# Kernel optimization log

Measured on AMD Instinct MI355X. Metric: run time of the kernel, lower is better.

Reference implementation:

```python
import jax, jax.numpy as jnp
import numpy as np

B, S, D, H, DFF = 2, 2048, 768, 12, 3072
HD = D // H
LN_EPS = 1e-5


def _layernorm(x, g, b):
    mu = jnp.mean(x, axis=-1, keepdims=True)
    var = jnp.mean((x - mu) ** 2, axis=-1, keepdims=True)
    return (x - mu) * jax.lax.rsqrt(var + LN_EPS) * g + b


def setup_inputs() -> dict:
    key = jax.random.key(0)
    ks = jax.random.split(key, 16)
    s_d = 1.0 / np.sqrt(D)
    s_ff = 1.0 / np.sqrt(DFF)
    return {
        "x": jax.random.normal(ks[0], (B, S, D), jnp.float32),
        "alibi_bias": jax.random.normal(ks[1], (H, S, S), jnp.float32) * 0.1,
        "Wq": jax.random.normal(ks[2], (D, D), jnp.float32) * s_d,
        "bq": jnp.zeros((D,), jnp.float32),
        "Wk": jax.random.normal(ks[3], (D, D), jnp.float32) * s_d,
        "bk": jnp.zeros((D,), jnp.float32),
        "Wv": jax.random.normal(ks[4], (D, D), jnp.float32) * s_d,
        "bv": jnp.zeros((D,), jnp.float32),
        "Wo": jax.random.normal(ks[5], (D, D), jnp.float32) * s_d,
        "bo": jnp.zeros((D,), jnp.float32),
        "W1": jax.random.normal(ks[6], (D, DFF), jnp.float32) * s_d,
        "b1": jnp.zeros((DFF,), jnp.float32),
        "W2": jax.random.normal(ks[7], (DFF, D), jnp.float32) * s_ff,
        "b2": jnp.zeros((D,), jnp.float32),
        "g1": jnp.ones((D,), jnp.float32),
        "be1": jnp.zeros((D,), jnp.float32),
        "g2": jnp.ones((D,), jnp.float32),
        "be2": jnp.zeros((D,), jnp.float32),
    }


def reference(x, alibi_bias, Wq, bq, Wk, bk, Wv, bv, Wo, bo, W1, b1, W2, b2, g1, be1, g2, be2):
    # QKV projections -> (B, H, S, HD)
    def split_heads(t):
        return t.reshape(B, S, H, HD).transpose(0, 2, 1, 3)

    q = split_heads(x @ Wq + bq)
    k = split_heads(x @ Wk + bk)
    v = split_heads(x @ Wv + bv)

    # causal mask (S, S): -inf above diagonal
    causal = jnp.where(jnp.triu(jnp.ones((S, S), bool), k=1), -jnp.inf, 0.0).astype(x.dtype)
    mask = alibi_bias[None] + causal[None, None]  # (1, H, S, S) broadcast over batch

    scale = 1.0 / np.sqrt(HD)
    scores = jnp.einsum("bhqd,bhkd->bhqk", q, k) * scale + mask
    probs = jax.nn.softmax(scores, axis=-1)
    attn = jnp.einsum("bhqk,bhkd->bhqd", probs, v)  # (B, H, S, HD)
    attn = attn.transpose(0, 2, 1, 3).reshape(B, S, D)
    attn = attn @ Wo + bo

    x = _layernorm(x + attn, g1, be1)
    ff = jax.nn.relu(x @ W1 + b1) @ W2 + b2
    x = _layernorm(x + ff, g2, be2)
    return x
```

## Files before the change

### kernel.cpp

```cpp
#include <hip/hip_runtime.h>
#include <hip/hip_bf16.h>

#define BB 2
#define SS 2048
#define DD 768
#define HH 12
#define HD 64
#define DFF 3072
#define NROW (BB * SS)
#define QLD  2304
#define LN_EPS 1e-5f

typedef __attribute__((ext_vector_type(8))) short bf16x8;
typedef __attribute__((ext_vector_type(4))) short bf16x4;
typedef __attribute__((ext_vector_type(4))) float f32x4;

__device__ __forceinline__ void gll16(const void* g, void* l) {
    __builtin_amdgcn_global_load_lds(
        (const __attribute__((address_space(1))) unsigned int*)g,
        (__attribute__((address_space(3))) unsigned int*)l,
        16, 0, 0);
}

__device__ __forceinline__ unsigned short bf16bits(float f) {
    __hip_bfloat16 h = __float2bfloat16(f);
    return *(unsigned short*)&h;
}

__device__ __forceinline__ float bf16tof(unsigned short u) {
    unsigned int ui = ((unsigned int)u) << 16;
    return __uint_as_float(ui);
}

__device__ __forceinline__ float block_sum(float v, float* red) {
    __syncthreads();
    #pragma unroll
    for (int off = 32; off > 0; off >>= 1) v += __shfl_down(v, off, 64);
    if ((threadIdx.x & 63) == 0) red[threadIdx.x >> 6] = v;
    __syncthreads();
    if (threadIdx.x == 0) red[0] = red[0] + red[1] + red[2] + red[3];
    __syncthreads();
    return red[0];
}

template<int TM, int TN>
__global__ __launch_bounds__(256) void mfma_gemm(
        const __hip_bfloat16* __restrict__ A, const __hip_bfloat16* __restrict__ BT,
        const float* __restrict__ bias, float* __restrict__ Cf,
        __hip_bfloat16* __restrict__ Cb,
        int N, int K, int relu, int bf16out, int qscale_cols) {
    constexpr int BK = 32;
    constexpr int MW = TM / 32;
    constexpr int NW = TN / 32;
    __shared__ __hip_bfloat16 a_s[TM * BK];
    __shared__ __hip_bfloat16 b_s[TN * BK];

    const int tid  = threadIdx.x;
    const int lane = tid & 63;
    const int wid  = tid >> 6;
    const int wm   = (wid & 1) * (TM / 2);
    const int wn   = (wid >> 1) * (TN / 2);
    const int qq   = lane & 15;
    const int quad = lane >> 4;
    const int m0 = blockIdx.y * TM;
    const int n0 = blockIdx.x * TN;

    const int srow = lane >> 2;
    const int scol = (lane & 3) * 8;

    f32x4 acc[MW][NW] = {};

    for (int k0 = 0; k0 < K; k0 += BK) {
        const __hip_bfloat16* Ag = A + (size_t)m0 * K + k0 + scol;
        #pragma unroll
        for (int i = 0; i < TM / 64; i++) {
            const int row = i * 64 + wid * 16 + srow;
            gll16(Ag + (size_t)row * K, a_s + row * BK + scol);
        }
        const __hip_bfloat16* Bg = BT + (size_t)n0 * K + k0 + scol;
        #pragma unroll
        for (int i = 0; i < TN / 64; i++) {
            const int row = i * 64 + wid * 16 + srow;
            gll16(Bg + (size_t)row * K, b_s + row * BK + scol);
        }
        __syncthreads();

        bf16x8 af[MW], bfr[NW];
        #pragma unroll
        for (int mi = 0; mi < MW; mi++)
            af[mi] = *(const bf16x8*)(a_s + (wm + mi * 16 + qq) * BK + quad * 8);
        #pragma unroll
        for (int ni = 0; ni < NW; ni++)
            bfr[ni] = *(const bf16x8*)(b_s + (wn + ni * 16 + qq) * BK + quad * 8);
        #pragma unroll
        for (int mi = 0; mi < MW; mi++)
            #pragma unroll
            for (int ni = 0; ni < NW; ni++)
                acc[mi][ni] = __builtin_amdgcn_mfma_f32_16x16x32_bf16(
                        af[mi], bfr[ni], acc[mi][ni], 0, 0, 0);
        __syncthreads();
    }

    #pragma unroll
    for (int mi = 0; mi < MW; mi++) {
        #pragma unroll
        for (int ni = 0; ni < NW; ni++) {
            const int col = n0 + wn + ni * 16 + qq;
            const float bv = bias[col];
            const float sc = (col < qscale_cols) ? 0.125f : 1.0f;
            #pragma unroll
            for (int r = 0; r < 4; r++) {
                const int row = m0 + wm + mi * 16 + quad * 4 + r;
                float v = acc[mi][ni][r] + bv;
                if (relu) v = fmaxf(v, 0.f);
                v *= sc;
                if (bf16out) Cb[(size_t)row * N + col] = __float2bfloat16(v);
                else         Cf[(size_t)row * N + col] = v;
            }
        }
    }
}

__global__ __launch_bounds__(256) void transpose_bf16_kernel(
        const float* __restrict__ in, __hip_bfloat16* __restrict__ out,
        int K, int N) {
    __shared__ float t[32][33];
    const int n0 = blockIdx.x * 32;
    const int k0 = blockIdx.y * 32;
    const int r = threadIdx.x >> 3;
    const int c = threadIdx.x & 7;
    float4 v = *(const float4*)&in[(size_t)(k0 + r) * N + n0 + c * 4];
    t[r][c * 4 + 0] = v.x;
    t[r][c * 4 + 1] = v.y;
    t[r][c * 4 + 2] = v.z;
    t[r][c * 4 + 3] = v.w;
    __syncthreads();
    union { unsigned short u[4]; uint2 w; } pk;
    #pragma unroll
    for (int j = 0; j < 4; j++) pk.u[j] = bf16bits(t[c * 4 + j][r]);
    *(uint2*)&out[(size_t)(n0 + r) * K + k0 + c * 4] = pk.w;
}

__global__ __launch_bounds__(256) void cvt_bf16_kernel(
        const float* __restrict__ in, __hip_bfloat16* __restrict__ out) {
    const int i = blockIdx.x * 256 + threadIdx.x;
    float4 v = ((const float4*)in)[i];
    union { unsigned short u[4]; uint2 w; } pk;
    pk.u[0] = bf16bits(v.x); pk.u[1] = bf16bits(v.y);
    pk.u[2] = bf16bits(v.z); pk.u[3] = bf16bits(v.w);
    ((uint2*)out)[i] = pk.w;
}

__global__ __launch_bounds__(256) void concat_bias_kernel(
        const float* __restrict__ bq, const float* __restrict__ bk,
        const float* __restrict__ bv, float* __restrict__ o) {
    const int i = blockIdx.x * 256 + threadIdx.x;
    if (i < QLD)
        o[i] = (i < DD) ? bq[i] : ((i < 2 * DD) ? bk[i - DD] : bv[i - 2 * DD]);
}

__global__ __launch_bounds__(256) void flash_attn_kernel(
        const __hip_bfloat16* __restrict__ QKV, const float* __restrict__ alibi,
        __hip_bfloat16* __restrict__ Opart, float* __restrict__ ml) {
    const int qt = (int)(gridDim.x >> 1) - 1 - (int)(blockIdx.x >> 1);
    const int s  = blockIdx.x & 1;
    const int h  = blockIdx.y;
    const int b  = blockIdx.z;
    const int tid  = threadIdx.x;
    const int lane = tid & 63;
    const int w    = tid >> 6;
    const int qq   = lane & 15;
    const int quad = lane >> 4;
    const int q0   = qt * 64;

    __shared__ unsigned short K_s[64 * 72];
    __shared__ unsigned short V_t[64 * 72];
    __shared__ unsigned short al_q[64 * 72];
    __shared__ unsigned short P_t[4][16 * 72];

    const size_t qrow = ((size_t)(b * SS + q0 + w * 16 + qq)) * QLD + (size_t)h * HD;
    const bf16x8 qf0 = *(const bf16x8*)(QKV + qrow + quad * 8);
    const bf16x8 qf1 = *(const bf16x8*)(QKV + qrow + 32 + quad * 8);

    f32x4 O[4] = {};
    float m_i = -1e30f, l_i = 0.f;

    const float* alrow = alibi + ((size_t)h * SS + q0) * SS;
    const size_t kvrow0 = (size_t)(b * SS) * QLD + (size_t)h * HD + w * 16;
    const int lim = q0 + w * 16 + qq;

    for (int t = s; t * 64 <= q0; t += 2) {
        const int k0 = t * 64;
        __syncthreads();

        {
            const size_t kv = kvrow0 + (size_t)(k0 + lane) * QLD;
            bf16x8 kv0 = *(const bf16x8*)(QKV + DD + kv);
            bf16x8 kv1 = *(const bf16x8*)(QKV + DD + kv + 8);
            *(bf16x8*)&K_s[lane * 72 + w * 16]     = kv0;
            *(bf16x8*)&K_s[lane * 72 + w * 16 + 8] = kv1;
            bf16x8 vv0 = *(const bf16x8*)(QKV + 2 * DD + kv);
            bf16x8 vv1 = *(const bf16x8*)(QKV + 2 * DD + kv + 8);
            #pragma unroll
            for (int j = 0; j < 8; j++) {
                V_t[(w * 16 + j) * 72 + lane]     = vv0[j];
                V_t[(w * 16 + 8 + j) * 72 + lane] = vv1[j];
            }
            const float* ap = alrow + (size_t)lane * SS + k0 + w * 16;
            union { unsigned short u[8]; bf16x8 v; } pa0, pa1;
            float4 f0 = *(const float4*)(ap);
            float4 f1 = *(const float4*)(ap + 4);
            float4 f2 = *(const float4*)(ap + 8);
            float4 f3 = *(const float4*)(ap + 12);
            pa0.u[0] = bf16bits(f0.x); pa0.u[1] = bf16bits(f0.y);
            pa0.u[2] = bf16bits(f0.z); pa0.u[3] = bf16bits(f0.w);
            pa0.u[4] = bf16bits(f1.x); pa0.u[5] = bf16bits(f1.y);
            pa0.u[6] = bf16bits(f1.z); pa0.u[7] = bf16bits(f1.w);
            pa1.u[0] = bf16bits(f2.x); pa1.u[1] = bf16bits(f2.y);
            pa1.u[2] = bf16bits(f2.z); pa1.u[3] = bf16bits(f2.w);
            pa1.u[4] = bf16bits(f3.x); pa1.u[5] = bf16bits(f3.y);
            pa1.u[6] = bf16bits(f3.z); pa1.u[7] = bf16bits(f3.w);
            *(bf16x8*)&al_q[lane * 72 + w * 16]     = pa0.v;
            *(bf16x8*)&al_q[lane * 72 + w * 16 + 8] = pa1.v;
        }
        __syncthreads();

        f32x4 S[4];
        #pragma unroll
        for (int c = 0; c < 4; c++) {
            f32x4 sacc = {};
            bf16x8 kf0 = *(const bf16x8*)&K_s[(c * 16 + qq) * 72 + quad * 8];
            bf16x8 kf1 = *(const bf16x8*)&K_s[(c * 16 + qq) * 72 + 32 + quad * 8];
            sacc = __builtin_amdgcn_mfma_f32_16x16x32_bf16(kf0, qf0, sacc, 0, 0, 0);
            sacc = __builtin_amdgcn_mfma_f32_16x16x32_bf16(kf1, qf1, sacc, 0, 0, 0);
            S[c] = sacc;
        }

        float sv[16];
        float smax = -1e30f;
        const int klim = lim - k0;
        #pragma unroll
        for (int c = 0; c < 4; c++) {
            bf16x4 a4 = *(const bf16x4*)&al_q[(w * 16 + qq) * 72 + c * 16 + quad * 4];
            #pragma unroll
            for (int r = 0; r < 4; r++) {
                const int key = c * 16 + quad * 4 + r;
                float sc = S[c][r] + bf16tof((unsigned short)a4[r]);
                if (key > klim) sc = -1e30f;
                sv[c * 4 + r] = sc;
                smax = fmaxf(smax, sc);
            }
        }
        smax = fmaxf(smax, __shfl_xor(smax, 16));
        smax = fmaxf(smax, __shfl_xor(smax, 32));

        const float nm = fmaxf(m_i, smax);
        const float alpha = __expf(m_i - nm);
        float lsum = 0.f;
        #pragma unroll
        for (int i = 0; i < 16; i++) {
            const float e = __expf(sv[i] - nm);
            sv[i] = e;
            lsum += e;
        }
        lsum += __shfl_xor(lsum, 16);
        lsum += __shfl_xor(lsum, 32);
        l_i = l_i * alpha + lsum;
        m_i = nm;

        #pragma unroll
        for (int c = 0; c < 4; c++) {
            bf16x4 pk;
            #pragma unroll
            for (int r = 0; r < 4; r++) pk[r] = (short)bf16bits(sv[c * 4 + r]);
            *(bf16x4*)&P_t[w][qq * 72 + c * 16 + quad * 4] = pk;
        }

        #pragma unroll
        for (int r = 0; r < 4; r++) {
            const float ar = __shfl(alpha, quad * 4 + r);
            #pragma unroll
            for (int d = 0; d < 4; d++) O[d][r] *= ar;
        }

        const bf16x8 pf0 = *(const bf16x8*)&P_t[w][qq * 72 + quad * 8];
        const bf16x8 pf1 = *(const bf16x8*)&P_t[w][qq * 72 + 32 + quad * 8];
        #pragma unroll
        for (int d0 = 0; d0 < 4; d0++) {
            bf16x8 vf0 = *(const bf16x8*)&V_t[(d0 * 16 + qq) * 72 + quad * 8];
            bf16x8 vf1 = *(const bf16x8*)&V_t[(d0 * 16 + qq) * 72 + 32 + quad * 8];
            O[d0] = __builtin_amdgcn_mfma_f32_16x16x32_bf16(pf0, vf0, O[d0], 0, 0, 0);
            O[d0] = __builtin_amdgcn_mfma_f32_16x16x32_bf16(pf1, vf1, O[d0], 0, 0, 0);
        }
    }

    if (quad == 0) {
        float* mlp = ml + (((size_t)(b * SS + q0 + w * 16 + qq) * HH + h) * 2 + s) * 2;
        mlp[0] = m_i;
        mlp[1] = l_i;
    }
    #pragma unroll
    for (int r = 0; r < 4; r++) {
        const int row = q0 + w * 16 + quad * 4 + r;
        __hip_bfloat16* op = Opart +
            (((size_t)(b * SS + row) * HH + h) * 2 + s) * 64 + qq;
        op[0]  = __float2bfloat16(O[0][r]);
        op[16] = __float2bfloat16(O[1][r]);
        op[32] = __float2bfloat16(O[2][r]);
        op[48] = __float2bfloat16(O[3][r]);
    }
}

__global__ __launch_bounds__(256) void attn_combine_kernel(
        const __hip_bfloat16* __restrict__ Opart, const float* __restrict__ ml,
        __hip_bfloat16* __restrict__ attnb) {
    const int idx = blockIdx.x * 256 + threadIdx.x;
    const int rr  = idx / 96;
    const int rem = idx - rr * 96;
    const int h   = rem >> 3;
    const int d8  = (rem & 7) * 8;
    const size_t base = ((size_t)rr * HH + h) * 2;
    const float m0 = ml[(base + 0) * 2], l0 = ml[(base + 0) * 2 + 1];
    const float m1 = ml[(base + 1) * 2], l1 = ml[(base + 1) * 2 + 1];
    const float m  = fmaxf(m0, m1);
    const float e0 = __expf(m0 - m);
    const float e1 = __expf(m1 - m);
    const float inv = 1.f / (l0 * e0 + l1 * e1);
    const bf16x8 o0 = *(const bf16x8*)(Opart + (base + 0) * 64 + d8);
    const bf16x8 o1 = *(const bf16x8*)(Opart + (base + 1) * 64 + d8);
    union { unsigned short u[8]; bf16x8 v; } pk;
    #pragma unroll
    for (int j = 0; j < 8; j++) {
        const float v = (bf16tof((unsigned short)o0[j]) * e0 +
                         bf16tof((unsigned short)o1[j]) * e1) * inv;
        pk.u[j] = bf16bits(v);
    }
    *(bf16x8*)(attnb + (size_t)rr * DD + h * 64 + d8) = pk.v;
}

__global__ __launch_bounds__(256) void ln_kernel(
        const float* __restrict__ a, const float* __restrict__ r,
        const float* __restrict__ g, const float* __restrict__ beta,
        float* __restrict__ outf, __hip_bfloat16* __restrict__ outb) {
    const int row = blockIdx.x;
    const int tid = threadIdx.x;
    __shared__ float red[64];

    float vals[3];
    float s = 0.f;
    #pragma unroll
    for (int i = 0; i < 3; i++) {
        const int col = i * 256 + tid;
        float t = a[(size_t)row * DD + col] + r[(size_t)row * DD + col];
        vals[i] = t;
        s += t;
    }
    const float mean = block_sum(s, red) * (1.f / DD);

    float s2 = 0.f;
    #pragma unroll
    for (int i = 0; i < 3; i++) {
        float d = vals[i] - mean;
        s2 += d * d;
    }
    const float var = block_sum(s2, red) * (1.f / DD);
    const float rstd = rsqrtf(var + LN_EPS);

    #pragma unroll
    for (int i = 0; i < 3; i++) {
        const int col = i * 256 + tid;
        const float o = (vals[i] - mean) * rstd * g[col] + beta[col];
        outf[(size_t)row * DD + col] = o;
        if (outb) outb[(size_t)row * DD + col] = __float2bfloat16(o);
    }
}

extern "C" void kernel_launch(void* const* d_in, const int* in_sizes, int n_in,
                              void* d_out, int out_size, void* d_ws, size_t ws_size,
                              hipStream_t stream) {
    const float* x     = (const float*)d_in[0];
    const float* alibi = (const float*)d_in[1];
    const float* Wq = (const float*)d_in[2];
    const float* bq = (const float*)d_in[3];
    const float* Wk = (const float*)d_in[4];
    const float* bk = (const float*)d_in[5];
    const float* Wv = (const float*)d_in[6];
    const float* bv = (const float*)d_in[7];
    const float* Wo = (const float*)d_in[8];
    const float* bo = (const float*)d_in[9];
    const float* W1 = (const float*)d_in[10];
    const float* b1 = (const float*)d_in[11];
    const float* W2 = (const float*)d_in[12];
    const float* b2 = (const float*)d_in[13];
    const float* g1 = (const float*)d_in[14];
    const float* be1 = (const float*)d_in[15];
    const float* g2 = (const float*)d_in[16];
    const float* be2 = (const float*)d_in[17];
    float* out = (float*)d_out;

    char* p = (char*)d_ws;
    auto alloc = [&](size_t bytes) { char* r = p; p += (bytes + 255) & ~(size_t)255; return r; };
    __hip_bfloat16* WqkvT = (__hip_bfloat16*)alloc((size_t)QLD * DD * 2);
    __hip_bfloat16* WoT   = (__hip_bfloat16*)alloc((size_t)DD * DD * 2);
    __hip_bfloat16* W1T   = (__hip_bfloat16*)alloc((size_t)DFF * DD * 2);
    __hip_bfloat16* W2T   = (__hip_bfloat16*)alloc((size_t)DD * DFF * 2);
    float*          biasc = (float*)alloc((size_t)QLD * 4);
    __hip_bfloat16* xb    = (__hip_bfloat16*)alloc((size_t)NROW * DD * 2);
    __hip_bfloat16* qkvb  = (__hip_bfloat16*)alloc((size_t)NROW * DFF * 2);
    __hip_bfloat16* attnb = (__hip_bfloat16*)alloc((size_t)NROW * DD * 2);
    float*          proj  = (float*)alloc((size_t)NROW * DD * 4);
    float*          ln1   = (float*)alloc((size_t)NROW * DD * 4);
    __hip_bfloat16* ln1b  = xb;
    __hip_bfloat16* ff1b  = qkvb;
    float*          ff2   = proj;

    __hip_bfloat16* Opart = (__hip_bfloat16*)proj;
    float*          mlbuf = (float*)xb;

    const dim3 blk(256);

    transpose_bf16_kernel<<<dim3(DD / 32, DD / 32), blk, 0, stream>>>(Wq, WqkvT, DD, DD);
    transpose_bf16_kernel<<<dim3(DD / 32, DD / 32), blk, 0, stream>>>(Wk, WqkvT + (size_t)DD * DD, DD, DD);
    transpose_bf16_kernel<<<dim3(DD / 32, DD / 32), blk, 0, stream>>>(Wv, WqkvT + (size_t)2 * DD * DD, DD, DD);
    transpose_bf16_kernel<<<dim3(DD / 32, DD / 32), blk, 0, stream>>>(Wo, WoT, DD, DD);
    transpose_bf16_kernel<<<dim3(DFF / 32, DD / 32), blk, 0, stream>>>(W1, W1T, DD, DFF);
    transpose_bf16_kernel<<<dim3(DD / 32, DFF / 32), blk, 0, stream>>>(W2, W2T, DFF, DD);
    concat_bias_kernel<<<dim3((QLD + 255) / 256), blk, 0, stream>>>(bq, bk, bv, biasc);
    cvt_bf16_kernel<<<dim3(NROW * DD / 4 / 256), blk, 0, stream>>>(x, xb);

    mfma_gemm<128, 128><<<dim3(QLD / 128, NROW / 128), blk, 0, stream>>>(
            xb, WqkvT, biasc, nullptr, qkvb, QLD, DD, 0, 1, DD);

    flash_attn_kernel<<<dim3(2 * (SS / 64), HH, BB), blk, 0, stream>>>(
            qkvb, alibi, Opart, mlbuf);
    attn_combine_kernel<<<dim3(NROW * 96 / 256), blk, 0, stream>>>(
            Opart, mlbuf, attnb);

    mfma_gemm<128, 64><<<dim3(DD / 64, NROW / 128), blk, 0, stream>>>(
            attnb, WoT, bo, proj, nullptr, DD, DD, 0, 0, 0);

    ln_kernel<<<dim3(NROW), blk, 0, stream>>>(x, proj, g1, be1, ln1, ln1b);

    mfma_gemm<128, 128><<<dim3(DFF / 128, NROW / 128), blk, 0, stream>>>(
            ln1b, W1T, b1, nullptr, ff1b, DFF, DD, 1, 1, 0);
    mfma_gemm<128, 64><<<dim3(DD / 64, NROW / 128), blk, 0, stream>>>(
            ff1b, W2T, b2, ff2, nullptr, DD, DFF, 0, 0, 0);

    ln_kernel<<<dim3(NROW), blk, 0, stream>>>(ln1, ff2, g2, be2, out, nullptr);
}
```

Baseline: 557.3 us.

## Split flash attention KV loop four ways and fuse prep kernels into one launch

The causal flash-attention KV loop is now split into four interleaved partitions instead of two, with the combine kernel generalized to merge NSPLIT partial outputs. The goal is more parallel blocks and shorter per-block tails for the long causal rows. The weight transposes, bias concat and x-to-bf16 conversion are also merged into a single prep kernel to remove launch overhead. In exchange, the partial-output buffer doubles in size and now spills past the proj scratch buffer it aliases, so correctness depends on the following allocation being contiguous. The combine kernel also gains extra memory traffic.

```diff
diff --git a/kernel.cpp b/kernel.cpp
--- a/kernel.cpp
+++ b/kernel.cpp
@@ -10,6 +10,7 @@
 #define NROW (BB * SS)
 #define QLD  2304
 #define LN_EPS 1e-5f
+#define NSPLIT 4
 
 typedef __attribute__((ext_vector_type(8))) short bf16x8;
 typedef __attribute__((ext_vector_type(4))) short bf16x4;
@@ -121,12 +122,11 @@
     }
 }
 
-__global__ __launch_bounds__(256) void transpose_bf16_kernel(
+__device__ __forceinline__ void transpose_tile(
         const float* __restrict__ in, __hip_bfloat16* __restrict__ out,
-        int K, int N) {
-    __shared__ float t[32][33];
-    const int n0 = blockIdx.x * 32;
-    const int k0 = blockIdx.y * 32;
+        int K, int N, int tix, int tiy, float (*t)[33]) {
+    const int n0 = tix * 32;
+    const int k0 = tiy * 32;
     const int r = threadIdx.x >> 3;
     const int c = threadIdx.x & 7;
     float4 v = *(const float4*)&in[(size_t)(k0 + r) * N + n0 + c * 4];
@@ -141,29 +141,48 @@
     *(uint2*)&out[(size_t)(n0 + r) * K + k0 + c * 4] = pk.w;
 }
 
-__global__ __launch_bounds__(256) void cvt_bf16_kernel(
-        const float* __restrict__ in, __hip_bfloat16* __restrict__ out) {
-    const int i = blockIdx.x * 256 + threadIdx.x;
-    float4 v = ((const float4*)in)[i];
-    union { unsigned short u[4]; uint2 w; } pk;
-    pk.u[0] = bf16bits(v.x); pk.u[1] = bf16bits(v.y);
-    pk.u[2] = bf16bits(v.z); pk.u[3] = bf16bits(v.w);
-    ((uint2*)out)[i] = pk.w;
-}
-
-__global__ __launch_bounds__(256) void concat_bias_kernel(
+__global__ __launch_bounds__(256) void prep_kernel(
+        const float* __restrict__ Wq, const float* __restrict__ Wk,
+        const float* __restrict__ Wv, const float* __restrict__ Wo,
+        const float* __restrict__ W1, const float* __restrict__ W2,
         const float* __restrict__ bq, const float* __restrict__ bk,
-        const float* __restrict__ bv, float* __restrict__ o) {
-    const int i = blockIdx.x * 256 + threadIdx.x;
-    if (i < QLD)
-        o[i] = (i < DD) ? bq[i] : ((i < 2 * DD) ? bk[i - DD] : bv[i - 2 * DD]);
+        const float* __restrict__ bv, const float* __restrict__ x,
+        __hip_bfloat16* __restrict__ WqkvT, __hip_bfloat16* __restrict__ WoT,
+        __hip_bfloat16* __restrict__ W1T, __hip_bfloat16* __restrict__ W2T,
+        float* __restrict__ biasc, __hip_bfloat16* __restrict__ xb) {
+    __shared__ float t[32][33];
+    const int bx = blockIdx.x;
+    if (bx < 2304) {
+        const int wsel = bx / 576;
+        const int r = bx - wsel * 576;
+        const float* in = (wsel == 0) ? Wq : (wsel == 1) ? Wk : (wsel == 2) ? Wv : Wo;
+        __hip_bfloat16* out = (wsel == 3) ? WoT : WqkvT + (size_t)wsel * DD * DD;
+        transpose_tile(in, out, DD, DD, r % 24, r / 24, t);
+    } else if (bx < 4608) {
+        const int r = bx - 2304;
+        transpose_tile(W1, W1T, DD, DFF, r % 96, r / 96, t);
+    } else if (bx < 6912) {
+        const int r = bx - 4608;
+        transpose_tile(W2, W2T, DFF, DD, r % 24, r / 24, t);
+    } else if (bx < 9984) {
+        const int i = (bx - 6912) * 256 + threadIdx.x;
+        float4 v = ((const float4*)x)[i];
+        union { unsigned short u[4]; uint2 w; } pk;
+        pk.u[0] = bf16bits(v.x); pk.u[1] = bf16bits(v.y);
+        pk.u[2] = bf16bits(v.z); pk.u[3] = bf16bits(v.w);
+        ((uint2*)xb)[i] = pk.w;
+    } else {
+        const int i = (bx - 9984) * 256 + threadIdx.x;
+        if (i < QLD)
+            biasc[i] = (i < DD) ? bq[i] : ((i < 2 * DD) ? bk[i - DD] : bv[i - 2 * DD]);
+    }
 }
 
 __global__ __launch_bounds__(256) void flash_attn_kernel(
         const __hip_bfloat16* __restrict__ QKV, const float* __restrict__ alibi,
         __hip_bfloat16* __restrict__ Opart, float* __restrict__ ml) {
-    const int qt = (int)(gridDim.x >> 1) - 1 - (int)(blockIdx.x >> 1);
-    const int s  = blockIdx.x & 1;
+    const int qt = (int)(gridDim.x >> 2) - 1 - (int)(blockIdx.x >> 2);
+    const int s  = blockIdx.x & 3;
     const int h  = blockIdx.y;
     const int b  = blockIdx.z;
     const int tid  = threadIdx.x;
@@ -189,7 +208,7 @@
     const size_t kvrow0 = (size_t)(b * SS) * QLD + (size_t)h * HD + w * 16;
     const int lim = q0 + w * 16 + qq;
 
-    for (int t = s; t * 64 <= q0; t += 2) {
+    for (int t = s; t * 64 <= q0; t += NSPLIT) {
         const int k0 = t * 64;
         __syncthreads();
 
@@ -295,7 +314,7 @@
     }
 
     if (quad == 0) {
-        float* mlp = ml + (((size_t)(b * SS + q0 + w * 16 + qq) * HH + h) * 2 + s) * 2;
+        float* mlp = ml + (((size_t)(b * SS + q0 + w * 16 + qq) * HH + h) * NSPLIT + s) * 2;
         mlp[0] = m_i;
         mlp[1] = l_i;
     }
@@ -303,7 +322,7 @@
     for (int r = 0; r < 4; r++) {
         const int row = q0 + w * 16 + quad * 4 + r;
         __hip_bfloat16* op = Opart +
-            (((size_t)(b * SS + row) * HH + h) * 2 + s) * 64 + qq;
+            (((size_t)(b * SS + row) * HH + h) * NSPLIT + s) * 64 + qq;
         op[0]  = __float2bfloat16(O[0][r]);
         op[16] = __float2bfloat16(O[1][r]);
         op[32] = __float2bfloat16(O[2][r]);
@@ -319,22 +338,33 @@
     const int rem = idx - rr * 96;
     const int h   = rem >> 3;
     const int d8  = (rem & 7) * 8;
-    const size_t base = ((size_t)rr * HH + h) * 2;
-    const float m0 = ml[(base + 0) * 2], l0 = ml[(base + 0) * 2 + 1];
-    const float m1 = ml[(base + 1) * 2], l1 = ml[(base + 1) * 2 + 1];
-    const float m  = fmaxf(m0, m1);
-    const float e0 = __expf(m0 - m);
-    const float e1 = __expf(m1 - m);
-    const float inv = 1.f / (l0 * e0 + l1 * e1);
-    const bf16x8 o0 = *(const bf16x8*)(Opart + (base + 0) * 64 + d8);
-    const bf16x8 o1 = *(const bf16x8*)(Opart + (base + 1) * 64 + d8);
+    const size_t base = ((size_t)rr * HH + h) * NSPLIT;
+    float ms[NSPLIT], ls[NSPLIT];
+    float m = -1e30f;
+    #pragma unroll
+    for (int s = 0; s < NSPLIT; s++) {
+        ms[s] = ml[(base + s) * 2];
+        ls[s] = ml[(base + s) * 2 + 1];
+        m = fmaxf(m, ms[s]);
+    }
+    float es[NSPLIT], denom = 0.f;
+    #pragma unroll
+    for (int s = 0; s < NSPLIT; s++) {
+        es[s] = __expf(ms[s] - m);
+        denom += ls[s] * es[s];
+    }
+    const float inv = 1.f / denom;
+    float acc[8] = {};
+    #pragma unroll
+    for (int s = 0; s < NSPLIT; s++) {
+        const bf16x8 o = *(const bf16x8*)(Opart + (base + s) * 64 + d8);
+        #pragma unroll
+        for (int j = 0; j < 8; j++)
+            acc[j] += bf16tof((unsigned short)o[j]) * es[s];
+    }
     union { unsigned short u[8]; bf16x8 v; } pk;
     #pragma unroll
-    for (int j = 0; j < 8; j++) {
-        const float v = (bf16tof((unsigned short)o0[j]) * e0 +
-                         bf16tof((unsigned short)o1[j]) * e1) * inv;
-        pk.u[j] = bf16bits(v);
-    }
+    for (int j = 0; j < 8; j++) pk.u[j] = bf16bits(acc[j] * inv);
     *(bf16x8*)(attnb + (size_t)rr * DD + h * 64 + d8) = pk.v;
 }
 
@@ -419,19 +449,14 @@
 
     const dim3 blk(256);
 
-    transpose_bf16_kernel<<<dim3(DD / 32, DD / 32), blk, 0, stream>>>(Wq, WqkvT, DD, DD);
-    transpose_bf16_kernel<<<dim3(DD / 32, DD / 32), blk, 0, stream>>>(Wk, WqkvT + (size_t)DD * DD, DD, DD);
-    transpose_bf16_kernel<<<dim3(DD / 32, DD / 32), blk, 0, stream>>>(Wv, WqkvT + (size_t)2 * DD * DD, DD, DD);
-    transpose_bf16_kernel<<<dim3(DD / 32, DD / 32), blk, 0, stream>>>(Wo, WoT, DD, DD);
-    transpose_bf16_kernel<<<dim3(DFF / 32, DD / 32), blk, 0, stream>>>(W1, W1T, DD, DFF);
-    transpose_bf16_kernel<<<dim3(DD / 32, DFF / 32), blk, 0, stream>>>(W2, W2T, DFF, DD);
-    concat_bias_kernel<<<dim3((QLD + 255) / 256), blk, 0, stream>>>(bq, bk, bv, biasc);
-    cvt_bf16_kernel<<<dim3(NROW * DD / 4 / 256), blk, 0, stream>>>(x, xb);
+    prep_kernel<<<dim3(9993), blk, 0, stream>>>(
+            Wq, Wk, Wv, Wo, W1, W2, bq, bk, bv, x,
+            WqkvT, WoT, W1T, W2T, biasc, xb);
 
     mfma_gemm<128, 128><<<dim3(QLD / 128, NROW / 128), blk, 0, stream>>>(
             xb, WqkvT, biasc, nullptr, qkvb, QLD, DD, 0, 1, DD);
 
-    flash_attn_kernel<<<dim3(2 * (SS / 64), HH, BB), blk, 0, stream>>>(
+    flash_attn_kernel<<<dim3(NSPLIT * (SS / 64), HH, BB), blk, 0, stream>>>(
             qkvb, alibi, Opart, mlbuf);
     attn_combine_kernel<<<dim3(NROW * 96 / 256), blk, 0, stream>>>(
             Opart, mlbuf, attnb);
```

Result: faster. 539.9 us (-3.1%).
